# Kernel optimization log

Measured on AMD Instinct MI355X. Metric: run time of the kernel, lower is better.

## Reference

```python
import jax, jax.numpy as jnp
import numpy as np

NTYPES = 2
B, N, MNEI = 4, 512, 100
M = MNEI * NTYPES          # neighbor slots = maxNeighborNum * ntypes
EMB_LAST = 100             # embedding net sizes [25, 50, 100]
FIT_H = 240
M2 = 16
RMIN, RMAX = 0.5, 6.0


def setup_inputs():
    key = jax.random.key(0)
    ks = jax.random.split(key, 24)
    r = jax.random.uniform(ks[0], (B, N, M), minval=0.6, maxval=7.0)
    v = jax.random.normal(ks[1], (B, N, M, 3))
    v = v / jnp.linalg.norm(v, axis=-1, keepdims=True)
    keep = jax.random.uniform(ks[2], (B, N, M)) < 0.7
    ImageDR = jnp.concatenate([r[..., None], r[..., None] * v], axis=-1)
    ImageDR = jnp.where(keep[..., None], ImageDR, 0.0).astype(jnp.float32)
    Imagetype_map = jax.random.randint(ks[3], (N,), 0, NTYPES)
    list_neigh = jax.random.randint(ks[4], (B, N, M), 0, N + 1)
    type_map = jnp.arange(NTYPES)
    davg = (0.01 * jax.random.normal(ks[5], (NTYPES, M, 4))).astype(jnp.float32)
    dstd = (1.0 + 0.1 * jax.random.uniform(ks[6], (NTYPES, M, 4))).astype(jnp.float32)

    def w(k, shape, fan):
        return (jax.random.normal(k, shape) / np.sqrt(fan)).astype(jnp.float32)

    def b(k, shape):
        return (0.1 * jax.random.normal(k, shape)).astype(jnp.float32)

    emb_W0 = w(ks[7], (NTYPES, NTYPES, 1, 25), 1)
    emb_b0 = b(ks[8], (NTYPES, NTYPES, 25))
    emb_W1 = w(ks[9], (NTYPES, NTYPES, 25, 50), 25)
    emb_b1 = b(ks[10], (NTYPES, NTYPES, 50))
    emb_W2 = w(ks[11], (NTYPES, NTYPES, 50, 100), 50)
    emb_b2 = b(ks[12], (NTYPES, NTYPES, 100))
    fin = M2 * EMB_LAST
    fit_W0 = w(ks[13], (NTYPES, fin, FIT_H), fin)
    fit_b0 = b(ks[14], (NTYPES, FIT_H))
    fit_W1 = w(ks[15], (NTYPES, FIT_H, FIT_H), FIT_H)
    fit_b1 = b(ks[16], (NTYPES, FIT_H))
    fit_W2 = w(ks[17], (NTYPES, FIT_H, FIT_H), FIT_H)
    fit_b2 = b(ks[18], (NTYPES, FIT_H))
    fit_W3 = w(ks[19], (NTYPES, FIT_H, 1), FIT_H)
    fit_b3 = b(ks[20], (NTYPES, 1))
    energy_shift = jnp.array([-3.37, -5.21], dtype=jnp.float32)
    return dict(list_neigh=list_neigh, Imagetype_map=Imagetype_map, type_map=type_map,
                ImageDR=ImageDR, nghost=0, davg=davg, dstd=dstd,
                emb_W0=emb_W0, emb_b0=emb_b0, emb_W1=emb_W1, emb_b1=emb_b1,
                emb_W2=emb_W2, emb_b2=emb_b2,
                fit_W0=fit_W0, fit_b0=fit_b0, fit_W1=fit_W1, fit_b1=fit_b1,
                fit_W2=fit_W2, fit_b2=fit_b2, fit_W3=fit_W3, fit_b3=fit_b3,
                energy_shift=energy_shift)


def _emb(s, W0, b0, W1, b1, W2, b2):
    # DeepPot-SE embedding net with doubling resnet connections
    h = jnp.tanh(s @ W0 + b0)                                   # [..., 25]
    h = jnp.tanh(h @ W1 + b1) + jnp.concatenate([h, h], -1)     # [..., 50]
    return jnp.tanh(h @ W2 + b2) + jnp.concatenate([h, h], -1)  # [..., 100]


def _fit(d, W0, b0, W1, b1, W2, b2, W3, b3):
    h = jnp.tanh(d @ W0 + b0)
    h = h + jnp.tanh(h @ W1 + b1)
    h = h + jnp.tanh(h @ W2 + b2)
    return h @ W3 + b3


def _forward(ImageDR, davg, dstd,
             emb_W0, emb_b0, emb_W1, emb_b1, emb_W2, emb_b2,
             fit_W0, fit_b0, fit_W1, fit_b1, fit_W2, fit_b2, fit_W3, fit_b3,
             energy_shift, Imagetype_map):
    Bsz, Nat, Mtot, _ = ImageDR.shape
    m = Mtot // NTYPES
    R = ImageDR[..., 0]
    Rsafe = jnp.where(R > 1e-5, R, 1.0)
    # smooth switching function s(r): 1/r below Rmin, polynomial taper to Rmax
    u = (R - RMIN) / (RMAX - RMIN)
    mid = (u ** 3 * (-6.0 * u * u + 15.0 * u - 10.0) + 1.0) / Rsafe
    S = jnp.where((R > 0) & (R < RMIN), 1.0 / Rsafe,
                  jnp.where((R > RMIN) & (R < RMAX), mid, 0.0))
    msk = (jnp.abs(R) > 1e-5)[..., None]
    Ri = jnp.concatenate([S[..., None],
                          jnp.where(msk, (S / Rsafe)[..., None] * ImageDR[..., 1:4], 0.0)],
                         axis=-1)                                    # [B,N,M,4] = (s, s*x/r, s*y/r, s*z/r)
    # per-center-type normalization (irregular gather of stats)
    Rn = (Ri - davg[Imagetype_map][None]) / dstd[Imagetype_map][None]
    tmask = [(Imagetype_map == i).astype(Rn.dtype)[None, :, None, None] for i in range(NTYPES)]
    xyz = jnp.zeros((Bsz, Nat, 4, EMB_LAST), Rn.dtype)
    for j in range(NTYPES):                                          # neighbor-type slice
        sl = Rn[:, :, j * m:(j + 1) * m, :]                          # [B,N,m,4]
        s = sl[..., 0:1]
        G = jnp.zeros(sl.shape[:3] + (EMB_LAST,), sl.dtype)
        for i in range(NTYPES):                                      # center type -> pair net (i, j)
            G = G + tmask[i] * _emb(s, emb_W0[i, j], emb_b0[i, j],
                                    emb_W1[i, j], emb_b1[i, j], emb_W2[i, j], emb_b2[i, j])
        xyz = xyz + jnp.einsum('bnmk,bnmc->bnkc', sl, G)
    xyz = xyz / (m * NTYPES)
    # descriptor D = (Ri^T G)^T (Ri^T G)[:, :M2], flattened -> [B,N,EMB_LAST*M2]
    D = jnp.einsum('bnkc,bnkd->bncd', xyz, xyz[..., :M2]).reshape(Bsz, Nat, -1)
    Ei = jnp.zeros((Bsz, Nat), D.dtype)
    for i in range(NTYPES):
        e = _fit(D, fit_W0[i], fit_b0[i], fit_W1[i], fit_b1[i],
                 fit_W2[i], fit_b2[i], fit_W3[i], fit_b3[i])[..., 0] + energy_shift[i]
        Ei = Ei + tmask[i][:, :, 0, 0] * e
    Etot = jnp.sum(Ei, axis=1)
    return Etot, Ei


def reference(list_neigh, Imagetype_map, type_map, ImageDR, nghost, davg, dstd,
              emb_W0, emb_b0, emb_W1, emb_b1, emb_W2, emb_b2,
              fit_W0, fit_b0, fit_W1, fit_b1, fit_W2, fit_b2, fit_W3, fit_b3,
              energy_shift):
    return _forward(ImageDR, davg, dstd,
                    emb_W0, emb_b0, emb_W1, emb_b1, emb_W2, emb_b2,
                    fit_W0, fit_b0, fit_W1, fit_b1, fit_W2, fit_b2, fit_W3, fit_b3,
                    energy_shift, Imagetype_map)
```

## Files before the change

### kernel.cpp

```cpp
#include <hip/hip_runtime.h>
#include <math.h>

#define NT 2
#define BSZ 4
#define NAT 512
#define NATOMS 2048
#define NNEI 200
#define EMB 100
#define FITH 240
#define DDIM 1600
#define TBK 1024

#define BIAS_F  16
#define W3C_F   (BIAS_F + 3 * 512)
#define PERM_I  2064
#define CNT_I   (PERM_I + 2048)
#define USH_BYTE 16512
#define TBL_U   0
#define W0T_U   409600
#define W1T_U   (W0T_U + 819200)
#define W2T_U   (W1T_U + 262144)
#define D_U     (W2T_U + 262144)
#define H0_U    (D_U + 3276800)
#define H1_U    (H0_U + 1048576)
#define USH_END (H1_U + 1048576)
#define WS_NEED ((size_t)USH_BYTE + (size_t)USH_END * 2)

#define N_W0 819200
#define N_W1 262144
#define N_W2 262144
#define N_B  1536
#define N_W3 512
#define N_EI 2048
#define N_WT (N_W0 + N_W1 + N_W2 + N_B + N_W3 + N_EI)
#define WT_BLK ((N_WT + 255) / 256)
#define TB_BLK 512

#define HPAD 264

typedef short s8v __attribute__((ext_vector_type(8)));
typedef float f4v __attribute__((ext_vector_type(4)));

__device__ __forceinline__ float ftanh(float x) {
    float ax = fabsf(x);
    float e = __expf(2.0f * ax);
    float t = 1.0f - __fdividef(2.0f, e + 1.0f);
    return (x < 0.0f) ? -t : t;
}
__device__ __forceinline__ unsigned short f2bf(float f) {
    unsigned u = __float_as_uint(f);
    u += 0x7FFFu + ((u >> 16) & 1u);
    return (unsigned short)(u >> 16);
}
__device__ __forceinline__ float bf2f(unsigned short s) {
    return __uint_as_float(((unsigned)s) << 16);
}
__device__ __forceinline__ float calc_S(float R) {
    float Rsafe = (R > 1e-5f) ? R : 1.0f;
    float u = (R - 0.5f) * (1.0f / 5.5f);
    float uu = u * u;
    float mid = (u * uu * (-6.0f * uu + 15.0f * u - 10.0f) + 1.0f) / Rsafe;
    float S = 0.0f;
    if (R > 0.0f && R < 0.5f)      S = 1.0f / Rsafe;
    else if (R > 0.5f && R < 6.0f) S = mid;
    return S;
}

__global__ void __launch_bounds__(256) prep_kernel(
    const float* __restrict__ fW0, const float* __restrict__ fW1,
    const float* __restrict__ fW2,
    const float* __restrict__ fb0, const float* __restrict__ fb1,
    const float* __restrict__ fb2,
    const float* __restrict__ fW3, const float* __restrict__ fb3,
    const float* __restrict__ eshift,
    const float* __restrict__ davg, const float* __restrict__ dstd,
    const float* __restrict__ eW0, const float* __restrict__ eb0,
    const float* __restrict__ eW1, const float* __restrict__ eb1,
    const float* __restrict__ eW2, const float* __restrict__ eb2,
    const int* __restrict__ itype,
    float* __restrict__ ws, float* __restrict__ out)
{
    __shared__ float los[100], his[100];
    __shared__ float rng[2];
    __shared__ float h0s[8][25];
    __shared__ float h1s[8][50];
    __shared__ int pcnt, poff0, poff1;
    const int tid = threadIdx.x;
    int bxg = blockIdx.x;
    unsigned short* u0 = (unsigned short*)((char*)ws + USH_BYTE);

    if (bxg < WT_BLK) {
        int id = bxg * 256 + tid;
        if (id < N_W0) {
            int n = id / 1600, k = id - n * 1600;
            float v = 0.0f;
            if (n < 240)                  v = fW0[(size_t)k * 240 + n];
            else if (n >= 256 && n < 496) v = fW0[(size_t)(1600 + k) * 240 + (n - 256)];
            u0[W0T_U + id] = f2bf(v);
            return;
        }
        id -= N_W0;
        if (id < N_W1) {
            int n = id / 512, k = id - n * 512;
            float v = 0.0f;
            if (n < 240 && k < 240)       v = fW1[(size_t)k * 240 + n];
            else if (n >= 256 && n < 496 && k >= 256 && k < 496)
                                          v = fW1[(size_t)(240 + (k - 256)) * 240 + (n - 256)];
            u0[W1T_U + id] = f2bf(v);
            return;
        }
        id -= N_W1;
        if (id < N_W2) {
            int n = id / 512, k = id - n * 512;
            float v = 0.0f;
            if (n < 240 && k < 240)       v = fW2[(size_t)k * 240 + n];
            else if (n >= 256 && n < 496 && k >= 256 && k < 496)
                                          v = fW2[(size_t)(240 + (k - 256)) * 240 + (n - 256)];
            u0[W2T_U + id] = f2bf(v);
            return;
        }
        id -= N_W2;
        if (id < N_B) {
            int l = id / 512, n = id - l * 512;
            const float* fb = (l == 0) ? fb0 : (l == 1) ? fb1 : fb2;
            float v = 0.0f;
            if (n < 240)                  v = fb[n];
            else if (n >= 256 && n < 496) v = fb[240 + (n - 256)];
            ws[BIAS_F + l * 512 + n] = v;
            return;
        }
        id -= N_B;
        if (id < N_W3) {
            int n = id;
            float v = 0.0f;
            if (n < 240)                  v = fW3[n];
            else if (n >= 256 && n < 496) v = fW3[240 + (n - 256)];
            ws[W3C_F + n] = v;
            return;
        }
        id -= N_W3;
        if (id < N_EI) {
            int t = itype[id & (NAT - 1)];
            out[4 + id] = fb3[t] + eshift[t];
        }
        return;
    }
    bxg -= WT_BLK;
    if (bxg < TB_BLK) {
        const int nid = bxg >> 7;
        const int kb  = (bxg & 127) * 8;
        const int t = nid >> 1, j = nid & 1;
        if (tid < 100) {
            int m = j * 100 + tid;
            float av = davg[(t * NNEI + m) * 4];
            float sd = dstd[(t * NNEI + m) * 4];
            float inv = __fdividef(1.0f, sd);
            float a = (0.0f - av) * inv;
            float b = (2.0f - av) * inv;
            los[tid] = fminf(a, b);
            his[tid] = fmaxf(a, b);
        }
        __syncthreads();
        if (tid == 0) {
            float lo = los[0], hi = his[0];
            for (int i = 1; i < 100; ++i) { lo = fminf(lo, los[i]); hi = fmaxf(hi, his[i]); }
            rng[0] = lo; rng[1] = hi - lo;
            if (kb == 0) {
                ws[nid * 2] = lo;
                ws[nid * 2 + 1] = (float)(TBK - 1) / (hi - lo);
            }
        }
        __syncthreads();
        const float smin = rng[0], span = rng[1];
        const float* W0 = eW0 + nid * 25;
        const float* B0 = eb0 + nid * 25;
        if (tid < 200) {
            int q = tid / 25, a = tid % 25;
            float s = smin + span * ((float)(kb + q) * (1.0f / (TBK - 1)));
            h0s[q][a] = ftanh(fmaf(s, W0[a], B0[a]));
        }
        __syncthreads();
        const float* W1 = eW1 + nid * 1250;
        const float* B1 = eb1 + nid * 50;
        for (int idx = tid; idx < 400; idx += 256) {
            int q = idx / 50, cc = idx % 50;
            float acc = B1[cc];
#pragma unroll
            for (int a = 0; a < 25; ++a) acc = fmaf(h0s[q][a], W1[a * 50 + cc], acc);
            h1s[q][cc] = ftanh(acc) + h0s[q][(cc < 25) ? cc : cc - 25];
        }
        __syncthreads();
        const float* W2 = eW2 + nid * 5000;
        const float* B2 = eb2 + nid * 100;
        unsigned short* tblu = u0 + TBL_U;
        for (int idx = tid; idx < 800; idx += 256) {
            int q = idx / 100, c = idx % 100;
            float acc = B2[c];
#pragma unroll
            for (int a = 0; a < 50; ++a) acc = fmaf(h1s[q][a], W2[a * 100 + c], acc);
            float g = ftanh(acc) + h1s[q][(c < 50) ? c : c - 50];
            tblu[(size_t)(nid * TBK + kb + q) * 100 + c] = f2bf(g);
        }
        return;
    }
    if (tid == 0) { pcnt = 0; poff0 = 0; poff1 = 0; }
    __syncthreads();
    int* wsi = (int*)ws;
    int local0 = 0;
    for (int i = tid; i < NATOMS; i += 256) local0 += (itype[i & (NAT - 1)] == 0);
    atomicAdd(&pcnt, local0);
    __syncthreads();
    const int c0 = pcnt;
    for (int i = tid; i < NATOMS; i += 256) {
        int t = itype[i & (NAT - 1)];
        int pos = (t == 0) ? atomicAdd(&poff0, 1) : (c0 + atomicAdd(&poff1, 1));
        wsi[PERM_I + pos] = i;
    }
    if (tid == 0) { wsi[CNT_I] = c0; wsi[CNT_I + 1] = NATOMS - c0; }
}

__global__ void __launch_bounds__(128) embed_kernel(
    const int* __restrict__ itype, const float* __restrict__ imagedr,
    const float* __restrict__ davg, const float* __restrict__ dstd,
    float* __restrict__ ws)
{
    __shared__ __align__(16) float4 srn[NNEI];
    __shared__ float sx[NNEI];
    __shared__ float part[2][400];
    const int atom = blockIdx.x;
    const int n = atom & (NAT - 1);
    const int tid = threadIdx.x;
    const int t = itype[n];
    unsigned short* u0 = (unsigned short*)((char*)ws + USH_BYTE);

    const float sm0 = ws[(t * 2 + 0) * 2], sc0 = ws[(t * 2 + 0) * 2 + 1];
    const float sm1 = ws[(t * 2 + 1) * 2], sc1 = ws[(t * 2 + 1) * 2 + 1];

    for (int m = tid; m < NNEI; m += 128) {
        float4 dr = ((const float4*)imagedr)[(size_t)atom * NNEI + m];
        float R = dr.x;
        float S = calc_S(R);
        float Rsafe = (R > 1e-5f) ? R : 1.0f;
        float sr = (fabsf(R) > 1e-5f) ? (S / Rsafe) : 0.0f;
        float4 av = ((const float4*)davg)[t * NNEI + m];
        float4 sd = ((const float4*)dstd)[t * NNEI + m];
        float4 rv;
        rv.x = (S         - av.x) / sd.x;
        rv.y = (sr * dr.y - av.y) / sd.y;
        rv.z = (sr * dr.z - av.z) / sd.z;
        rv.w = (sr * dr.w - av.w) / sd.w;
        srn[m] = rv;
        float smin = (m >= 100) ? sm1 : sm0;
        float scal = (m >= 100) ? sc1 : sc0;
        sx[m] = fminf(fmaxf((rv.x - smin) * scal, 0.0f), (float)(TBK - 2) + 0.9999f);
    }
    __syncthreads();

    const int w = tid >> 6, lane = tid & 63;
    const unsigned short* T = u0 + TBL_U + (size_t)(t * 2 + w) * TBK * EMB;
    const bool hi = (lane < 36);
    float xA0 = 0, xA1 = 0, xA2 = 0, xA3 = 0;
    float xB0 = 0, xB1 = 0, xB2 = 0, xB3 = 0;
#pragma unroll 4
    for (int mi = 0; mi < 100; ++mi) {
        int m = w * 100 + mi;
        float4 rv = srn[m];
        float x = sx[m];
        int i = (int)x;
        float f = x - (float)i;
        const unsigned short* Tr = T + (size_t)i * EMB;
        float g0 = bf2f(Tr[lane]);
        float g1 = bf2f(Tr[EMB + lane]);
        float g = fmaf(f, g1 - g0, g0);
        xA0 = fmaf(rv.x, g, xA0); xA1 = fmaf(rv.y, g, xA1);
        xA2 = fmaf(rv.z, g, xA2); xA3 = fmaf(rv.w, g, xA3);
        if (hi) {
            float h0v = bf2f(Tr[64 + lane]);
            float h1v = bf2f(Tr[EMB + 64 + lane]);
            float g2 = fmaf(f, h1v - h0v, h0v);
            xB0 = fmaf(rv.x, g2, xB0); xB1 = fmaf(rv.y, g2, xB1);
            xB2 = fmaf(rv.z, g2, xB2); xB3 = fmaf(rv.w, g2, xB3);
        }
    }
    part[w][0 * 100 + lane] = xA0; part[w][1 * 100 + lane] = xA1;
    part[w][2 * 100 + lane] = xA2; part[w][3 * 100 + lane] = xA3;
    if (hi) {
        part[w][0 * 100 + 64 + lane] = xB0; part[w][1 * 100 + 64 + lane] = xB1;
        part[w][2 * 100 + 64 + lane] = xB2; part[w][3 * 100 + 64 + lane] = xB3;
    }
    __syncthreads();
    const float inv = 1.0f / 200.0f;
    for (int idx = tid; idx < 400; idx += 128)
        part[0][idx] = (part[0][idx] + part[1][idx]) * inv;
    __syncthreads();
    unsigned short* Drow = u0 + D_U + (size_t)atom * DDIM;
    const float* xt = part[0];
    for (int idx = tid; idx < DDIM; idx += 128) {
        int c = idx >> 4, d = idx & 15;
        float s = xt[c] * xt[d] + xt[100 + c] * xt[100 + d]
                + xt[200 + c] * xt[200 + d] + xt[300 + c] * xt[300 + d];
        Drow[idx] = f2bf(s);
    }
}

__device__ __forceinline__ void fit_gemm256(
    const unsigned short* Hsrc, const unsigned short* Bp,
    int h, int mr, int q, f4v acc[4])
{
#pragma unroll
    for (int kt = 0; kt < 4; ++kt) {
        s8v av = *(const s8v*)((const char*)Hsrc
                 + (size_t)mr * (HPAD * 2) + h * 256 + q * 16 + kt * 64);
#pragma unroll
        for (int j = 0; j < 4; ++j) {
            s8v b = *(const s8v*)(Bp + j * 16 * 512 + kt * 32);
            acc[j] = __builtin_amdgcn_mfma_f32_16x16x32_bf16(av, b, acc[j], 0, 0, 0);
        }
    }
}

__global__ void __launch_bounds__(512) fit_kernel(
    const unsigned short* __restrict__ A,
    const unsigned short* __restrict__ W0T,
    const unsigned short* __restrict__ W1T,
    const unsigned short* __restrict__ W2T,
    const float* __restrict__ biases,
    const float* __restrict__ w3c,
    const int* __restrict__ wsi,
    float* __restrict__ out)
{
    __shared__ float lred[4][64][17];
    __shared__ unsigned short Hs0[16 * HPAD];
    __shared__ unsigned short Hs1[16 * HPAD];
    __shared__ float red2[16][4];

    const int z = blockIdx.y;
    const int cnt = wsi[CNT_I + z];
    const int my = blockIdx.x;
    if (my * 16 >= cnt) return;
    const int base = z ? wsi[CNT_I] : 0;
    const int tid = threadIdx.x;
    const int w = tid >> 6, lane = tid & 63;
    const int mr = lane & 15, q = lane >> 4;
    const int wc = w & 3, h = w >> 2;
    const int n0 = z * 256 + wc * 64;
    const int m0 = my * 16;
    const int arow = wsi[PERM_I + base + min(m0 + mr, cnt - 1)];

    {
        const unsigned short* Ap = A   + (size_t)arow * DDIM + h * 800 + q * 8;
        const unsigned short* Bp = W0T + (size_t)(n0 + mr) * DDIM + h * 800 + q * 8;
        f4v a0 = {0,0,0,0}, a1 = {0,0,0,0}, a2 = {0,0,0,0}, a3 = {0,0,0,0};
#pragma unroll 5
        for (int kt = 0; kt < 25; ++kt) {
            s8v av = *(const s8v*)(Ap + kt * 32);
            s8v b0 = *(const s8v*)(Bp + kt * 32);
            s8v b1 = *(const s8v*)(Bp + 16 * DDIM + kt * 32);
            s8v b2 = *(const s8v*)(Bp + 32 * DDIM + kt * 32);
            s8v b3 = *(const s8v*)(Bp + 48 * DDIM + kt * 32);
            a0 = __builtin_amdgcn_mfma_f32_16x16x32_bf16(av, b0, a0, 0, 0, 0);
            a1 = __builtin_amdgcn_mfma_f32_16x16x32_bf16(av, b1, a1, 0, 0, 0);
            a2 = __builtin_amdgcn_mfma_f32_16x16x32_bf16(av, b2, a2, 0, 0, 0);
            a3 = __builtin_amdgcn_mfma_f32_16x16x32_bf16(av, b3, a3, 0, 0, 0);
        }
        if (h == 1) {
#pragma unroll
            for (int r = 0; r < 4; ++r) {
                lred[wc][lane][r]      = a0[r];
                lred[wc][lane][4 + r]  = a1[r];
                lred[wc][lane][8 + r]  = a2[r];
                lred[wc][lane][12 + r] = a3[r];
            }
        }
        __syncthreads();
        if (h == 0) {
#pragma unroll
            for (int j = 0; j < 4; ++j) {
                const float bv = biases[n0 + j * 16 + mr];
                f4v* ap = (j == 0) ? &a0 : (j == 1) ? &a1 : (j == 2) ? &a2 : &a3;
#pragma unroll
                for (int r = 0; r < 4; ++r) {
                    float s = (*ap)[r] + lred[wc][lane][j * 4 + r] + bv;
                    int row = q * 4 + r, col = wc * 64 + j * 16 + mr;
                    Hs0[row * HPAD + col] = f2bf(ftanh(s));
                }
            }
        }
        __syncthreads();
    }

    {
        const unsigned short* Bp = W1T + (size_t)(n0 + mr) * 512 + z * 256 + h * 128 + q * 8;
        f4v acc[4] = {{0,0,0,0},{0,0,0,0},{0,0,0,0},{0,0,0,0}};
        fit_gemm256(Hs0, Bp, h, mr, q, acc);
        if (h == 1) {
#pragma unroll
            for (int j = 0; j < 4; ++j)
#pragma unroll
                for (int r = 0; r < 4; ++r) lred[wc][lane][j * 4 + r] = acc[j][r];
        }
        __syncthreads();
        if (h == 0) {
#pragma unroll
            for (int j = 0; j < 4; ++j) {
                const float bv = biases[512 + n0 + j * 16 + mr];
#pragma unroll
                for (int r = 0; r < 4; ++r) {
                    float s = acc[j][r] + lred[wc][lane][j * 4 + r] + bv;
                    int row = q * 4 + r, col = wc * 64 + j * 16 + mr;
                    float hv = bf2f(Hs0[row * HPAD + col]) + ftanh(s);
                    Hs1[row * HPAD + col] = f2bf(hv);
                }
            }
        }
        __syncthreads();
    }

    {
        const unsigned short* Bp = W2T + (size_t)(n0 + mr) * 512 + z * 256 + h * 128 + q * 8;
        f4v acc[4] = {{0,0,0,0},{0,0,0,0},{0,0,0,0},{0,0,0,0}};
        fit_gemm256(Hs1, Bp, h, mr, q, acc);
        if (h == 1) {
#pragma unroll
            for (int j = 0; j < 4; ++j)
#pragma unroll
                for (int r = 0; r < 4; ++r) lred[wc][lane][j * 4 + r] = acc[j][r];
        }
        __syncthreads();
        if (h == 0) {
            float pr[4] = {0, 0, 0, 0};
#pragma unroll
            for (int j = 0; j < 4; ++j) {
                const int col = n0 + j * 16 + mr;
                const float bv = biases[1024 + col];
                const float wv = w3c[col];
#pragma unroll
                for (int r = 0; r < 4; ++r) {
                    float s = acc[j][r] + lred[wc][lane][j * 4 + r] + bv;
                    int row = q * 4 + r, coll = wc * 64 + j * 16 + mr;
                    float hv = bf2f(Hs1[row * HPAD + coll]) + ftanh(s);
                    pr[r] = fmaf(hv, wv, pr[r]);
                }
            }
#pragma unroll
            for (int r = 0; r < 4; ++r) {
                float p = pr[r];
                p += __shfl_xor(p, 1, 16);
                p += __shfl_xor(p, 2, 16);
                p += __shfl_xor(p, 4, 16);
                p += __shfl_xor(p, 8, 16);
                if (mr == 0) red2[q * 4 + r][wc] = p;
            }
        }
        __syncthreads();
        if (tid < 16 && m0 + tid < cnt) {
            const int orow = wsi[PERM_I + base + m0 + tid];
            out[4 + orow] += red2[tid][0] + red2[tid][1] + red2[tid][2] + red2[tid][3];
        }
    }
}

__global__ void etot_kernel(float* __restrict__ out) {
    const int b = blockIdx.x;
    float s = 0.0f;
    for (int n = threadIdx.x; n < NAT; n += 256) s += out[4 + b * NAT + n];
#pragma unroll
    for (int off = 32; off > 0; off >>= 1) s += __shfl_down(s, off, 64);
    __shared__ float rr[4];
    if ((threadIdx.x & 63) == 0) rr[threadIdx.x >> 6] = s;
    __syncthreads();
    if (threadIdx.x == 0) out[b] = rr[0] + rr[1] + rr[2] + rr[3];
}

__global__ void dp_atom_kernel(
    const int* __restrict__ itype, const float* __restrict__ imagedr,
    const float* __restrict__ davg, const float* __restrict__ dstd,
    const float* __restrict__ eW0, const float* __restrict__ eb0,
    const float* __restrict__ eW1, const float* __restrict__ eb1,
    const float* __restrict__ eW2, const float* __restrict__ eb2,
    const float* __restrict__ fW0, const float* __restrict__ fb0,
    const float* __restrict__ fW1, const float* __restrict__ fb1,
    const float* __restrict__ fW2, const float* __restrict__ fb2,
    const float* __restrict__ fW3, const float* __restrict__ fb3,
    const float* __restrict__ eshift, float* __restrict__ out)
{
    __shared__ __align__(16) float4 rn4[NNEI];
    __shared__ __align__(16) float  xyz[4 * EMB];
    __shared__ __align__(16) float  h0s[100 * 25];
    __shared__ __align__(16) float  smem[100 * 52];
    const int atom = blockIdx.x;
    const int n = atom & (NAT - 1);
    const int tid = threadIdx.x;
    const int t = itype[n];
    for (int m = tid; m < NNEI; m += 256) {
        float4 dr = ((const float4*)imagedr)[(size_t)atom * NNEI + m];
        float R = dr.x;
        float S = calc_S(R);
        float Rsafe = (R > 1e-5f) ? R : 1.0f;
        float sr = (fabsf(R) > 1e-5f) ? (S / Rsafe) : 0.0f;
        float4 av = ((const float4*)davg)[t * NNEI + m];
        float4 sd = ((const float4*)dstd)[t * NNEI + m];
        float4 rv;
        rv.x = (S - av.x) / sd.x; rv.y = (sr * dr.y - av.y) / sd.y;
        rv.z = (sr * dr.z - av.z) / sd.z; rv.w = (sr * dr.w - av.w) / sd.w;
        rn4[m] = rv;
    }
    const int c = tid & 127; const int mh = tid >> 7;
    float xp0 = 0, xp1 = 0, xp2 = 0, xp3 = 0;
    for (int j = 0; j < NT; ++j) {
        const int wb = t * NT + j;
        const float* W0 = eW0 + wb * 25; const float* B0 = eb0 + wb * 25;
        const float* W1 = eW1 + wb * 1250; const float* B1 = eb1 + wb * 50;
        const float* W2 = eW2 + wb * 5000; const float* B2 = eb2 + wb * 100;
        __syncthreads();
        for (int idx = tid; idx < 2500; idx += 256) {
            int m = idx / 25, a = idx - m * 25;
            h0s[idx] = ftanh(fmaf(rn4[j * 100 + m].x, W0[a], B0[a]));
        }
        __syncthreads();
        for (int idx = tid; idx < 5000; idx += 256) {
            int m = idx / 50, cc = idx - m * 50;
            const float* h0m = h0s + m * 25;
            float acc = B1[cc];
#pragma unroll
            for (int a = 0; a < 25; ++a) acc = fmaf(h0m[a], W1[a * 50 + cc], acc);
            smem[m * 52 + cc] = ftanh(acc) + h0m[(cc < 25) ? cc : cc - 25];
        }
        for (int idx = tid; idx < 200; idx += 256)
            smem[(idx >> 1) * 52 + 50 + (idx & 1)] = 0.0f;
        __syncthreads();
        if (c < EMB) {
            float w2c[52];
#pragma unroll
            for (int a = 0; a < 50; ++a) w2c[a] = W2[a * EMB + c];
            w2c[50] = 0; w2c[51] = 0;
            const float bc = B2[c];
            const int sk = (c < 50) ? c : c - 50;
            for (int i = 0; i < 50; ++i) {
                int m = mh * 50 + i;
                const float* h1m = smem + m * 52;
                float acc = bc;
#pragma unroll
                for (int q = 0; q < 13; ++q) {
                    float4 hv = ((const float4*)h1m)[q];
                    acc = fmaf(hv.x, w2c[4 * q], acc); acc = fmaf(hv.y, w2c[4 * q + 1], acc);
                    acc = fmaf(hv.z, w2c[4 * q + 2], acc); acc = fmaf(hv.w, w2c[4 * q + 3], acc);
                }
                float g = ftanh(acc) + h1m[sk];
                float4 rm = rn4[j * 100 + m];
                xp0 = fmaf(rm.x, g, xp0); xp1 = fmaf(rm.y, g, xp1);
                xp2 = fmaf(rm.z, g, xp2); xp3 = fmaf(rm.w, g, xp3);
            }
        }
    }
    __syncthreads();
    const float inv = 1.0f / 200.0f;
    if (mh == 0 && c < EMB) {
        xyz[c] = xp0 * inv; xyz[EMB + c] = xp1 * inv;
        xyz[2 * EMB + c] = xp2 * inv; xyz[3 * EMB + c] = xp3 * inv;
    }
    __syncthreads();
    if (mh == 1 && c < EMB) {
        xyz[c] += xp0 * inv; xyz[EMB + c] += xp1 * inv;
        xyz[2 * EMB + c] += xp2 * inv; xyz[3 * EMB + c] += xp3 * inv;
    }
    __syncthreads();
    float* Dld = smem;
    for (int idx = tid; idx < DDIM; idx += 256) {
        int cc = idx >> 4, d = idx & 15;
        Dld[idx] = xyz[cc] * xyz[d] + xyz[EMB + cc] * xyz[EMB + d]
                 + xyz[2 * EMB + cc] * xyz[2 * EMB + d] + xyz[3 * EMB + cc] * xyz[3 * EMB + d];
    }
    __syncthreads();
    float* hA = smem + DDIM; float* hB = hA + FITH; float* h2 = hB + FITH; float* red = h2 + FITH;
    if (tid < FITH) {
        const float* W = fW0 + (size_t)t * DDIM * FITH;
        float acc = fb0[t * FITH + tid];
        for (int f = 0; f < DDIM; f += 4) {
            float4 dv = *(const float4*)(Dld + f);
            acc = fmaf(dv.x, W[f * FITH + tid], acc); acc = fmaf(dv.y, W[(f + 1) * FITH + tid], acc);
            acc = fmaf(dv.z, W[(f + 2) * FITH + tid], acc); acc = fmaf(dv.w, W[(f + 3) * FITH + tid], acc);
        }
        hA[tid] = ftanh(acc);
    }
    __syncthreads();
    if (tid < FITH) {
        const float* W = fW1 + t * FITH * FITH;
        float acc = fb1[t * FITH + tid];
        for (int f = 0; f < FITH; f += 4) {
            float4 hv = *(const float4*)(hA + f);
            acc = fmaf(hv.x, W[f * FITH + tid], acc); acc = fmaf(hv.y, W[(f + 1) * FITH + tid], acc);
            acc = fmaf(hv.z, W[(f + 2) * FITH + tid], acc); acc = fmaf(hv.w, W[(f + 3) * FITH + tid], acc);
        }
        hB[tid] = hA[tid] + ftanh(acc);
    }
    __syncthreads();
    if (tid < FITH) {
        const float* W = fW2 + t * FITH * FITH;
        float acc = fb2[t * FITH + tid];
        for (int f = 0; f < FITH; f += 4) {
            float4 hv = *(const float4*)(hB + f);
            acc = fmaf(hv.x, W[f * FITH + tid], acc); acc = fmaf(hv.y, W[(f + 1) * FITH + tid], acc);
            acc = fmaf(hv.z, W[(f + 2) * FITH + tid], acc); acc = fmaf(hv.w, W[(f + 3) * FITH + tid], acc);
        }
        h2[tid] = hB[tid] + ftanh(acc);
    }
    __syncthreads();
    float p = (tid < FITH) ? h2[tid] * fW3[t * FITH + tid] : 0.0f;
#pragma unroll
    for (int off = 32; off > 0; off >>= 1) p += __shfl_down(p, off, 64);
    if ((tid & 63) == 0) red[tid >> 6] = p;
    __syncthreads();
    if (tid == 0) out[4 + atom] = red[0] + red[1] + red[2] + red[3] + fb3[t] + eshift[t];
}

extern "C" void kernel_launch(void* const* d_in, const int* in_sizes, int n_in,
                              void* d_out, int out_size, void* d_ws, size_t ws_size,
                              hipStream_t stream) {
    const int*   itype   = (const int*)  d_in[1];
    const float* imagedr = (const float*)d_in[3];
    const float* davg    = (const float*)d_in[5];
    const float* dstd    = (const float*)d_in[6];
    const float* eW0     = (const float*)d_in[7];
    const float* eb0     = (const float*)d_in[8];
    const float* eW1     = (const float*)d_in[9];
    const float* eb1     = (const float*)d_in[10];
    const float* eW2     = (const float*)d_in[11];
    const float* eb2     = (const float*)d_in[12];
    const float* fW0     = (const float*)d_in[13];
    const float* fb0     = (const float*)d_in[14];
    const float* fW1     = (const float*)d_in[15];
    const float* fb1     = (const float*)d_in[16];
    const float* fW2     = (const float*)d_in[17];
    const float* fb2     = (const float*)d_in[18];
    const float* fW3     = (const float*)d_in[19];
    const float* fb3     = (const float*)d_in[20];
    const float* eshift  = (const float*)d_in[21];
    float* out = (float*)d_out;
    float* ws  = (float*)d_ws;

    if (ws_size >= WS_NEED) {
        unsigned short* u0 = (unsigned short*)((char*)ws + USH_BYTE);
        const int* wsi = (const int*)ws;
        prep_kernel<<<WT_BLK + TB_BLK + 1, 256, 0, stream>>>(
            fW0, fW1, fW2, fb0, fb1, fb2, fW3, fb3, eshift,
            davg, dstd, eW0, eb0, eW1, eb1, eW2, eb2, itype, ws, out);
        embed_kernel<<<NATOMS, 128, 0, stream>>>(itype, imagedr, davg, dstd, ws);
        fit_kernel<<<dim3(128, 2), 512, 0, stream>>>(
            u0 + D_U, u0 + W0T_U, u0 + W1T_U, u0 + W2T_U,
            ws + BIAS_F, ws + W3C_F, wsi, out);
        etot_kernel<<<BSZ, 256, 0, stream>>>(out);
    } else {
        dp_atom_kernel<<<NATOMS, 256, 0, stream>>>(itype, imagedr, davg, dstd,
            eW0, eb0, eW1, eb1, eW2, eb2,
            fW0, fb0, fW1, fb1, fW2, fb2, fW3, fb3, eshift, out);
        etot_kernel<<<BSZ, 256, 0, stream>>>(out);
    }
}
```

Measured before the change: 193.7 us.

## Software-prefetch table and weight loads, halve fit row tile to double blocks

```diff
diff --git a/kernel.cpp b/kernel.cpp
--- a/kernel.cpp
+++ b/kernel.cpp
@@ -37,6 +37,8 @@
 #define TB_BLK 512
 
 #define HPAD 264
+#define PF 6
+#define PFE 6
 
 typedef short s8v __attribute__((ext_vector_type(8)));
 typedef float f4v __attribute__((ext_vector_type(4)));
@@ -261,22 +263,41 @@
     const bool hi = (lane < 36);
     float xA0 = 0, xA1 = 0, xA2 = 0, xA3 = 0;
     float xB0 = 0, xB1 = 0, xB2 = 0, xB3 = 0;
-#pragma unroll 4
+
+    float ff[PFE];
+    unsigned short cb[PFE][4];
+#pragma unroll
+    for (int p = 0; p < PFE; ++p) {
+        float x = sx[w * 100 + p];
+        int i = (int)x;
+        ff[p] = x - (float)i;
+        const unsigned short* Tr = T + (size_t)i * EMB;
+        cb[p][0] = Tr[lane];
+        cb[p][1] = Tr[EMB + lane];
+        cb[p][2] = Tr[64 + lane];
+        cb[p][3] = Tr[EMB + 64 + lane];
+    }
+#pragma unroll
     for (int mi = 0; mi < 100; ++mi) {
-        int m = w * 100 + mi;
-        float4 rv = srn[m];
-        float x = sx[m];
-        int i = (int)x;
-        float f = x - (float)i;
-        const unsigned short* Tr = T + (size_t)i * EMB;
-        float g0 = bf2f(Tr[lane]);
-        float g1 = bf2f(Tr[EMB + lane]);
+        const int s = mi % PFE;
+        float4 rv = srn[w * 100 + mi];
+        float f  = ff[s];
+        float g0 = bf2f(cb[s][0]), g1 = bf2f(cb[s][1]);
+        float h0v = bf2f(cb[s][2]), h1v = bf2f(cb[s][3]);
+        if (mi + PFE < 100) {
+            float x = sx[w * 100 + mi + PFE];
+            int i = (int)x;
+            ff[s] = x - (float)i;
+            const unsigned short* Tr = T + (size_t)i * EMB;
+            cb[s][0] = Tr[lane];
+            cb[s][1] = Tr[EMB + lane];
+            cb[s][2] = Tr[64 + lane];
+            cb[s][3] = Tr[EMB + 64 + lane];
+        }
         float g = fmaf(f, g1 - g0, g0);
         xA0 = fmaf(rv.x, g, xA0); xA1 = fmaf(rv.y, g, xA1);
         xA2 = fmaf(rv.z, g, xA2); xA3 = fmaf(rv.w, g, xA3);
         if (hi) {
-            float h0v = bf2f(Tr[64 + lane]);
-            float h1v = bf2f(Tr[EMB + 64 + lane]);
             float g2 = fmaf(f, h1v - h0v, h0v);
             xB0 = fmaf(rv.x, g2, xB0); xB1 = fmaf(rv.y, g2, xB1);
             xB2 = fmaf(rv.z, g2, xB2); xB3 = fmaf(rv.w, g2, xB3);
@@ -300,22 +321,6 @@
         float s = xt[c] * xt[d] + xt[100 + c] * xt[100 + d]
                 + xt[200 + c] * xt[200 + d] + xt[300 + c] * xt[300 + d];
         Drow[idx] = f2bf(s);
-    }
-}
-
-__device__ __forceinline__ void fit_gemm256(
-    const unsigned short* Hsrc, const unsigned short* Bp,
-    int h, int mr, int q, f4v acc[4])
-{
-#pragma unroll
-    for (int kt = 0; kt < 4; ++kt) {
-        s8v av = *(const s8v*)((const char*)Hsrc
-                 + (size_t)mr * (HPAD * 2) + h * 256 + q * 16 + kt * 64);
-#pragma unroll
-        for (int j = 0; j < 4; ++j) {
-            s8v b = *(const s8v*)(Bp + j * 16 * 512 + kt * 32);
-            acc[j] = __builtin_amdgcn_mfma_f32_16x16x32_bf16(av, b, acc[j], 0, 0, 0);
-        }
     }
 }
 
@@ -330,69 +335,108 @@
     float* __restrict__ out)
 {
     __shared__ float lred[4][64][17];
-    __shared__ unsigned short Hs0[16 * HPAD];
-    __shared__ unsigned short Hs1[16 * HPAD];
-    __shared__ float red2[16][4];
+    __shared__ unsigned short Hs0[8 * HPAD];
+    __shared__ unsigned short Hs1[8 * HPAD];
+    __shared__ float red2[8][4];
 
     const int z = blockIdx.y;
     const int cnt = wsi[CNT_I + z];
     const int my = blockIdx.x;
-    if (my * 16 >= cnt) return;
+    if (my * 8 >= cnt) return;
     const int base = z ? wsi[CNT_I] : 0;
     const int tid = threadIdx.x;
     const int w = tid >> 6, lane = tid & 63;
     const int mr = lane & 15, q = lane >> 4;
     const int wc = w & 3, h = w >> 2;
     const int n0 = z * 256 + wc * 64;
-    const int m0 = my * 16;
-    const int arow = wsi[PERM_I + base + min(m0 + mr, cnt - 1)];
-
+    const int m0 = my * 8;
+    const int arow = wsi[PERM_I + base + min(m0 + (mr & 7), cnt - 1)];
+
+    s8v abuf[PF];
+    s8v bbuf[PF][4];
+
+    f4v a0 = {0,0,0,0}, a1 = {0,0,0,0}, a2 = {0,0,0,0}, a3 = {0,0,0,0};
     {
         const unsigned short* Ap = A   + (size_t)arow * DDIM + h * 800 + q * 8;
         const unsigned short* Bp = W0T + (size_t)(n0 + mr) * DDIM + h * 800 + q * 8;
-        f4v a0 = {0,0,0,0}, a1 = {0,0,0,0}, a2 = {0,0,0,0}, a3 = {0,0,0,0};
-#pragma unroll 5
+#pragma unroll
+        for (int p = 0; p < PF; ++p) {
+            abuf[p] = *(const s8v*)(Ap + p * 32);
+#pragma unroll
+            for (int j = 0; j < 4; ++j)
+                bbuf[p][j] = *(const s8v*)(Bp + j * 16 * DDIM + p * 32);
+        }
+#pragma unroll
         for (int kt = 0; kt < 25; ++kt) {
-            s8v av = *(const s8v*)(Ap + kt * 32);
-            s8v b0 = *(const s8v*)(Bp + kt * 32);
-            s8v b1 = *(const s8v*)(Bp + 16 * DDIM + kt * 32);
-            s8v b2 = *(const s8v*)(Bp + 32 * DDIM + kt * 32);
-            s8v b3 = *(const s8v*)(Bp + 48 * DDIM + kt * 32);
+            const int s = kt % PF;
+            s8v av = abuf[s];
+            s8v b0 = bbuf[s][0], b1 = bbuf[s][1], b2 = bbuf[s][2], b3 = bbuf[s][3];
+            if (kt + PF < 25) {
+                abuf[s] = *(const s8v*)(Ap + (kt + PF) * 32);
+#pragma unroll
+                for (int j = 0; j < 4; ++j)
+                    bbuf[s][j] = *(const s8v*)(Bp + j * 16 * DDIM + (kt + PF) * 32);
+            }
             a0 = __builtin_amdgcn_mfma_f32_16x16x32_bf16(av, b0, a0, 0, 0, 0);
             a1 = __builtin_amdgcn_mfma_f32_16x16x32_bf16(av, b1, a1, 0, 0, 0);
             a2 = __builtin_amdgcn_mfma_f32_16x16x32_bf16(av, b2, a2, 0, 0, 0);
             a3 = __builtin_amdgcn_mfma_f32_16x16x32_bf16(av, b3, a3, 0, 0, 0);
         }
-        if (h == 1) {
+    }
+    {
+        const unsigned short* Bp1 = W1T + (size_t)(n0 + mr) * 512 + z * 256 + h * 128 + q * 8;
+#pragma unroll
+        for (int kt = 0; kt < 4; ++kt)
+#pragma unroll
+            for (int j = 0; j < 4; ++j)
+                bbuf[kt][j] = *(const s8v*)(Bp1 + j * 16 * 512 + kt * 32);
+    }
+    if (h == 1) {
+#pragma unroll
+        for (int r = 0; r < 4; ++r) {
+            lred[wc][lane][r]      = a0[r];
+            lred[wc][lane][4 + r]  = a1[r];
+            lred[wc][lane][8 + r]  = a2[r];
+            lred[wc][lane][12 + r] = a3[r];
+        }
+    }
+    __syncthreads();
+    if (h == 0) {
+#pragma unroll
+        for (int j = 0; j < 4; ++j) {
+            const float bv = biases[n0 + j * 16 + mr];
+            f4v* ap = (j == 0) ? &a0 : (j == 1) ? &a1 : (j == 2) ? &a2 : &a3;
 #pragma unroll
             for (int r = 0; r < 4; ++r) {
-                lred[wc][lane][r]      = a0[r];
-                lred[wc][lane][4 + r]  = a1[r];
-                lred[wc][lane][8 + r]  = a2[r];
-                lred[wc][lane][12 + r] = a3[r];
-            }
-        }
-        __syncthreads();
-        if (h == 0) {
-#pragma unroll
-            for (int j = 0; j < 4; ++j) {
-                const float bv = biases[n0 + j * 16 + mr];
-                f4v* ap = (j == 0) ? &a0 : (j == 1) ? &a1 : (j == 2) ? &a2 : &a3;
-#pragma unroll
-                for (int r = 0; r < 4; ++r) {
+                int row = q * 4 + r;
+                if (row < 8) {
                     float s = (*ap)[r] + lred[wc][lane][j * 4 + r] + bv;
-                    int row = q * 4 + r, col = wc * 64 + j * 16 + mr;
+                    int col = wc * 64 + j * 16 + mr;
                     Hs0[row * HPAD + col] = f2bf(ftanh(s));
                 }
             }
         }
-        __syncthreads();
-    }
+    }
+    __syncthreads();
 
     {
-        const unsigned short* Bp = W1T + (size_t)(n0 + mr) * 512 + z * 256 + h * 128 + q * 8;
         f4v acc[4] = {{0,0,0,0},{0,0,0,0},{0,0,0,0},{0,0,0,0}};
-        fit_gemm256(Hs0, Bp, h, mr, q, acc);
+#pragma unroll
+        for (int kt = 0; kt < 4; ++kt) {
+            s8v av = *(const s8v*)((const char*)Hs0
+                     + (size_t)(mr & 7) * (HPAD * 2) + h * 256 + q * 16 + kt * 64);
+#pragma unroll
+            for (int j = 0; j < 4; ++j)
+                acc[j] = __builtin_amdgcn_mfma_f32_16x16x32_bf16(av, bbuf[kt][j], acc[j], 0, 0, 0);
+        }
+        {
+            const unsigned short* Bp2 = W2T + (size_t)(n0 + mr) * 512 + z * 256 + h * 128 + q * 8;
+#pragma unroll
+            for (int kt = 0; kt < 4; ++kt)
+#pragma unroll
+                for (int j = 0; j < 4; ++j)
+                    bbuf[kt][j] = *(const s8v*)(Bp2 + j * 16 * 512 + kt * 32);
+        }
         if (h == 1) {
 #pragma unroll
             for (int j = 0; j < 4; ++j)
@@ -406,10 +450,13 @@
                 const float bv = biases[512 + n0 + j * 16 + mr];
 #pragma unroll
                 for (int r = 0; r < 4; ++r) {
-                    float s = acc[j][r] + lred[wc][lane][j * 4 + r] + bv;
-                    int row = q * 4 + r, col = wc * 64 + j * 16 + mr;
-                    float hv = bf2f(Hs0[row * HPAD + col]) + ftanh(s);
-                    Hs1[row * HPAD + col] = f2bf(hv);
+                    int row = q * 4 + r;
+                    if (row < 8) {
+                        float s = acc[j][r] + lred[wc][lane][j * 4 + r] + bv;
+                        int col = wc * 64 + j * 16 + mr;
+                        float hv = bf2f(Hs0[row * HPAD + col]) + ftanh(s);
+                        Hs1[row * HPAD + col] = f2bf(hv);
+                    }
                 }
             }
         }
@@ -417,9 +464,15 @@
     }
 
     {
-        const unsigned short* Bp = W2T + (size_t)(n0 + mr) * 512 + z * 256 + h * 128 + q * 8;
         f4v acc[4] = {{0,0,0,0},{0,0,0,0},{0,0,0,0},{0,0,0,0}};
-        fit_gemm256(Hs1, Bp, h, mr, q, acc);
+#pragma unroll
+        for (int kt = 0; kt < 4; ++kt) {
+            s8v av = *(const s8v*)((const char*)Hs1
+                     + (size_t)(mr & 7) * (HPAD * 2) + h * 256 + q * 16 + kt * 64);
+#pragma unroll
+            for (int j = 0; j < 4; ++j)
+                acc[j] = __builtin_amdgcn_mfma_f32_16x16x32_bf16(av, bbuf[kt][j], acc[j], 0, 0, 0);
+        }
         if (h == 1) {
 #pragma unroll
             for (int j = 0; j < 4; ++j)
@@ -427,7 +480,7 @@
                 for (int r = 0; r < 4; ++r) lred[wc][lane][j * 4 + r] = acc[j][r];
         }
         __syncthreads();
-        if (h == 0) {
+        if (h == 0 && q < 2) {
             float pr[4] = {0, 0, 0, 0};
 #pragma unroll
             for (int j = 0; j < 4; ++j) {
@@ -453,7 +506,7 @@
             }
         }
         __syncthreads();
-        if (tid < 16 && m0 + tid < cnt) {
+        if (tid < 8 && m0 + tid < cnt) {
             const int orow = wsi[PERM_I + base + m0 + tid];
             out[4 + orow] += red2[tid][0] + red2[tid][1] + red2[tid][2] + red2[tid][3];
         }
@@ -646,7 +699,7 @@
             fW0, fW1, fW2, fb0, fb1, fb2, fW3, fb3, eshift,
             davg, dstd, eW0, eb0, eW1, eb1, eW2, eb2, itype, ws, out);
         embed_kernel<<<NATOMS, 128, 0, stream>>>(itype, imagedr, davg, dstd, ws);
-        fit_kernel<<<dim3(128, 2), 512, 0, stream>>>(
+        fit_kernel<<<dim3(256, 2), 512, 0, stream>>>(
             u0 + D_U, u0 + W0T_U, u0 + W1T_U, u0 + W2T_U,
             ws + BIAS_F, ws + W3C_F, wsi, out);
         etot_kernel<<<BSZ, 256, 0, stream>>>(out);
```

Result: slower. 399.7 us (+106.3%).

## Process 32 atoms per fit block to reuse weight loads across two M-tiles

Applied to the files above, without the earlier changes.

```diff
diff --git a/kernel.cpp b/kernel.cpp
--- a/kernel.cpp
+++ b/kernel.cpp
@@ -303,22 +303,6 @@
     }
 }
 
-__device__ __forceinline__ void fit_gemm256(
-    const unsigned short* Hsrc, const unsigned short* Bp,
-    int h, int mr, int q, f4v acc[4])
-{
-#pragma unroll
-    for (int kt = 0; kt < 4; ++kt) {
-        s8v av = *(const s8v*)((const char*)Hsrc
-                 + (size_t)mr * (HPAD * 2) + h * 256 + q * 16 + kt * 64);
-#pragma unroll
-        for (int j = 0; j < 4; ++j) {
-            s8v b = *(const s8v*)(Bp + j * 16 * 512 + kt * 32);
-            acc[j] = __builtin_amdgcn_mfma_f32_16x16x32_bf16(av, b, acc[j], 0, 0, 0);
-        }
-    }
-}
-
 __global__ void __launch_bounds__(512) fit_kernel(
     const unsigned short* __restrict__ A,
     const unsigned short* __restrict__ W0T,
@@ -329,88 +313,120 @@
     const int* __restrict__ wsi,
     float* __restrict__ out)
 {
-    __shared__ float lred[4][64][17];
-    __shared__ unsigned short Hs0[16 * HPAD];
-    __shared__ unsigned short Hs1[16 * HPAD];
-    __shared__ float red2[16][4];
+    __shared__ float lred[4][64][33];
+    __shared__ unsigned short Hs[32 * HPAD];
+    __shared__ float red2[32][4];
 
     const int z = blockIdx.y;
     const int cnt = wsi[CNT_I + z];
     const int my = blockIdx.x;
-    if (my * 16 >= cnt) return;
+    if (my * 32 >= cnt) return;
     const int base = z ? wsi[CNT_I] : 0;
     const int tid = threadIdx.x;
     const int w = tid >> 6, lane = tid & 63;
     const int mr = lane & 15, q = lane >> 4;
     const int wc = w & 3, h = w >> 2;
     const int n0 = z * 256 + wc * 64;
-    const int m0 = my * 16;
-    const int arow = wsi[PERM_I + base + min(m0 + mr, cnt - 1)];
-
+    const int m0 = my * 32;
+    const int ar0 = wsi[PERM_I + base + min(m0 + mr, cnt - 1)];
+    const int ar1 = wsi[PERM_I + base + min(m0 + 16 + mr, cnt - 1)];
+
+    f4v acc[2][4] = {{{0,0,0,0},{0,0,0,0},{0,0,0,0},{0,0,0,0}},
+                     {{0,0,0,0},{0,0,0,0},{0,0,0,0},{0,0,0,0}}};
     {
-        const unsigned short* Ap = A   + (size_t)arow * DDIM + h * 800 + q * 8;
+        const unsigned short* Ap0 = A + (size_t)ar0 * DDIM + h * 800 + q * 8;
+        const unsigned short* Ap1 = A + (size_t)ar1 * DDIM + h * 800 + q * 8;
         const unsigned short* Bp = W0T + (size_t)(n0 + mr) * DDIM + h * 800 + q * 8;
-        f4v a0 = {0,0,0,0}, a1 = {0,0,0,0}, a2 = {0,0,0,0}, a3 = {0,0,0,0};
 #pragma unroll 5
         for (int kt = 0; kt < 25; ++kt) {
-            s8v av = *(const s8v*)(Ap + kt * 32);
+            s8v av0 = *(const s8v*)(Ap0 + kt * 32);
+            s8v av1 = *(const s8v*)(Ap1 + kt * 32);
             s8v b0 = *(const s8v*)(Bp + kt * 32);
             s8v b1 = *(const s8v*)(Bp + 16 * DDIM + kt * 32);
             s8v b2 = *(const s8v*)(Bp + 32 * DDIM + kt * 32);
             s8v b3 = *(const s8v*)(Bp + 48 * DDIM + kt * 32);
-            a0 = __builtin_amdgcn_mfma_f32_16x16x32_bf16(av, b0, a0, 0, 0, 0);
-            a1 = __builtin_amdgcn_mfma_f32_16x16x32_bf16(av, b1, a1, 0, 0, 0);
-            a2 = __builtin_amdgcn_mfma_f32_16x16x32_bf16(av, b2, a2, 0, 0, 0);
-            a3 = __builtin_amdgcn_mfma_f32_16x16x32_bf16(av, b3, a3, 0, 0, 0);
-        }
-        if (h == 1) {
-#pragma unroll
-            for (int r = 0; r < 4; ++r) {
-                lred[wc][lane][r]      = a0[r];
-                lred[wc][lane][4 + r]  = a1[r];
-                lred[wc][lane][8 + r]  = a2[r];
-                lred[wc][lane][12 + r] = a3[r];
-            }
-        }
-        __syncthreads();
-        if (h == 0) {
-#pragma unroll
-            for (int j = 0; j < 4; ++j) {
-                const float bv = biases[n0 + j * 16 + mr];
-                f4v* ap = (j == 0) ? &a0 : (j == 1) ? &a1 : (j == 2) ? &a2 : &a3;
+            acc[0][0] = __builtin_amdgcn_mfma_f32_16x16x32_bf16(av0, b0, acc[0][0], 0, 0, 0);
+            acc[0][1] = __builtin_amdgcn_mfma_f32_16x16x32_bf16(av0, b1, acc[0][1], 0, 0, 0);
+            acc[0][2] = __builtin_amdgcn_mfma_f32_16x16x32_bf16(av0, b2, acc[0][2], 0, 0, 0);
+            acc[0][3] = __builtin_amdgcn_mfma_f32_16x16x32_bf16(av0, b3, acc[0][3], 0, 0, 0);
+            acc[1][0] = __builtin_amdgcn_mfma_f32_16x16x32_bf16(av1, b0, acc[1][0], 0, 0, 0);
+            acc[1][1] = __builtin_amdgcn_mfma_f32_16x16x32_bf16(av1, b1, acc[1][1], 0, 0, 0);
+            acc[1][2] = __builtin_amdgcn_mfma_f32_16x16x32_bf16(av1, b2, acc[1][2], 0, 0, 0);
+            acc[1][3] = __builtin_amdgcn_mfma_f32_16x16x32_bf16(av1, b3, acc[1][3], 0, 0, 0);
+        }
+    }
+    if (h == 1) {
+#pragma unroll
+        for (int g = 0; g < 2; ++g)
+#pragma unroll
+            for (int j = 0; j < 4; ++j)
+#pragma unroll
+                for (int r = 0; r < 4; ++r)
+                    lred[wc][lane][g * 16 + j * 4 + r] = acc[g][j][r];
+    }
+    __syncthreads();
+    if (h == 0) {
+#pragma unroll
+        for (int j = 0; j < 4; ++j) {
+            const float bv = biases[n0 + j * 16 + mr];
+            const int col = wc * 64 + j * 16 + mr;
+#pragma unroll
+            for (int g = 0; g < 2; ++g)
 #pragma unroll
                 for (int r = 0; r < 4; ++r) {
-                    float s = (*ap)[r] + lred[wc][lane][j * 4 + r] + bv;
-                    int row = q * 4 + r, col = wc * 64 + j * 16 + mr;
-                    Hs0[row * HPAD + col] = f2bf(ftanh(s));
+                    float s = acc[g][j][r] + lred[wc][lane][g * 16 + j * 4 + r] + bv;
+                    int row = g * 16 + q * 4 + r;
+                    Hs[row * HPAD + col] = f2bf(ftanh(s));
                 }
-            }
-        }
-        __syncthreads();
-    }
+        }
+    }
+    __syncthreads();
 
     {
         const unsigned short* Bp = W1T + (size_t)(n0 + mr) * 512 + z * 256 + h * 128 + q * 8;
-        f4v acc[4] = {{0,0,0,0},{0,0,0,0},{0,0,0,0},{0,0,0,0}};
-        fit_gemm256(Hs0, Bp, h, mr, q, acc);
+        f4v ac1[2][4] = {{{0,0,0,0},{0,0,0,0},{0,0,0,0},{0,0,0,0}},
+                         {{0,0,0,0},{0,0,0,0},{0,0,0,0},{0,0,0,0}}};
+#pragma unroll
+        for (int kt = 0; kt < 4; ++kt) {
+            s8v av0 = *(const s8v*)((const char*)Hs + (size_t)mr * (HPAD * 2) + h * 256 + q * 16 + kt * 64);
+            s8v av1 = *(const s8v*)((const char*)Hs + (size_t)(16 + mr) * (HPAD * 2) + h * 256 + q * 16 + kt * 64);
+            s8v b0 = *(const s8v*)(Bp + kt * 32);
+            s8v b1 = *(const s8v*)(Bp + 16 * 512 + kt * 32);
+            s8v b2 = *(const s8v*)(Bp + 32 * 512 + kt * 32);
+            s8v b3 = *(const s8v*)(Bp + 48 * 512 + kt * 32);
+            ac1[0][0] = __builtin_amdgcn_mfma_f32_16x16x32_bf16(av0, b0, ac1[0][0], 0, 0, 0);
+            ac1[0][1] = __builtin_amdgcn_mfma_f32_16x16x32_bf16(av0, b1, ac1[0][1], 0, 0, 0);
+            ac1[0][2] = __builtin_amdgcn_mfma_f32_16x16x32_bf16(av0, b2, ac1[0][2], 0, 0, 0);
+            ac1[0][3] = __builtin_amdgcn_mfma_f32_16x16x32_bf16(av0, b3, ac1[0][3], 0, 0, 0);
+            ac1[1][0] = __builtin_amdgcn_mfma_f32_16x16x32_bf16(av1, b0, ac1[1][0], 0, 0, 0);
+            ac1[1][1] = __builtin_amdgcn_mfma_f32_16x16x32_bf16(av1, b1, ac1[1][1], 0, 0, 0);
+            ac1[1][2] = __builtin_amdgcn_mfma_f32_16x16x32_bf16(av1, b2, ac1[1][2], 0, 0, 0);
+            ac1[1][3] = __builtin_amdgcn_mfma_f32_16x16x32_bf16(av1, b3, ac1[1][3], 0, 0, 0);
+        }
         if (h == 1) {
 #pragma unroll
-            for (int j = 0; j < 4; ++j)
-#pragma unroll
-                for (int r = 0; r < 4; ++r) lred[wc][lane][j * 4 + r] = acc[j][r];
+            for (int g = 0; g < 2; ++g)
+#pragma unroll
+                for (int j = 0; j < 4; ++j)
+#pragma unroll
+                    for (int r = 0; r < 4; ++r)
+                        lred[wc][lane][g * 16 + j * 4 + r] = ac1[g][j][r];
         }
         __syncthreads();
         if (h == 0) {
 #pragma unroll
             for (int j = 0; j < 4; ++j) {
                 const float bv = biases[512 + n0 + j * 16 + mr];
-#pragma unroll
-                for (int r = 0; r < 4; ++r) {
-                    float s = acc[j][r] + lred[wc][lane][j * 4 + r] + bv;
-                    int row = q * 4 + r, col = wc * 64 + j * 16 + mr;
-                    float hv = bf2f(Hs0[row * HPAD + col]) + ftanh(s);
-                    Hs1[row * HPAD + col] = f2bf(hv);
-                }
+                const int col = wc * 64 + j * 16 + mr;
+#pragma unroll
+                for (int g = 0; g < 2; ++g)
+#pragma unroll
+                    for (int r = 0; r < 4; ++r) {
+                        float s = ac1[g][j][r] + lred[wc][lane][g * 16 + j * 4 + r] + bv;
+                        int row = g * 16 + q * 4 + r;
+                        float hv = bf2f(Hs[row * HPAD + col]) + ftanh(s);
+                        Hs[row * HPAD + col] = f2bf(hv);
+                    }
             }
         }
         __syncthreads();
@@ -418,42 +434,67 @@
 
     {
         const unsigned short* Bp = W2T + (size_t)(n0 + mr) * 512 + z * 256 + h * 128 + q * 8;
-        f4v acc[4] = {{0,0,0,0},{0,0,0,0},{0,0,0,0},{0,0,0,0}};
-        fit_gemm256(Hs1, Bp, h, mr, q, acc);
+        f4v ac2[2][4] = {{{0,0,0,0},{0,0,0,0},{0,0,0,0},{0,0,0,0}},
+                         {{0,0,0,0},{0,0,0,0},{0,0,0,0},{0,0,0,0}}};
+#pragma unroll
+        for (int kt = 0; kt < 4; ++kt) {
+            s8v av0 = *(const s8v*)((const char*)Hs + (size_t)mr * (HPAD * 2) + h * 256 + q * 16 + kt * 64);
+            s8v av1 = *(const s8v*)((const char*)Hs + (size_t)(16 + mr) * (HPAD * 2) + h * 256 + q * 16 + kt * 64);
+            s8v b0 = *(const s8v*)(Bp + kt * 32);
+            s8v b1 = *(const s8v*)(Bp + 16 * 512 + kt * 32);
+            s8v b2 = *(const s8v*)(Bp + 32 * 512 + kt * 32);
+            s8v b3 = *(const s8v*)(Bp + 48 * 512 + kt * 32);
+            ac2[0][0] = __builtin_amdgcn_mfma_f32_16x16x32_bf16(av0, b0, ac2[0][0], 0, 0, 0);
+            ac2[0][1] = __builtin_amdgcn_mfma_f32_16x16x32_bf16(av0, b1, ac2[0][1], 0, 0, 0);
+            ac2[0][2] = __builtin_amdgcn_mfma_f32_16x16x32_bf16(av0, b2, ac2[0][2], 0, 0, 0);
+            ac2[0][3] = __builtin_amdgcn_mfma_f32_16x16x32_bf16(av0, b3, ac2[0][3], 0, 0, 0);
+            ac2[1][0] = __builtin_amdgcn_mfma_f32_16x16x32_bf16(av1, b0, ac2[1][0], 0, 0, 0);
+            ac2[1][1] = __builtin_amdgcn_mfma_f32_16x16x32_bf16(av1, b1, ac2[1][1], 0, 0, 0);
+            ac2[1][2] = __builtin_amdgcn_mfma_f32_16x16x32_bf16(av1, b2, ac2[1][2], 0, 0, 0);
+            ac2[1][3] = __builtin_amdgcn_mfma_f32_16x16x32_bf16(av1, b3, ac2[1][3], 0, 0, 0);
+        }
         if (h == 1) {
 #pragma unroll
-            for (int j = 0; j < 4; ++j)
-#pragma unroll
-                for (int r = 0; r < 4; ++r) lred[wc][lane][j * 4 + r] = acc[j][r];
+            for (int g = 0; g < 2; ++g)
+#pragma unroll
+                for (int j = 0; j < 4; ++j)
+#pragma unroll
+                    for (int r = 0; r < 4; ++r)
+                        lred[wc][lane][g * 16 + j * 4 + r] = ac2[g][j][r];
         }
         __syncthreads();
         if (h == 0) {
-            float pr[4] = {0, 0, 0, 0};
+            float pr[2][4] = {{0, 0, 0, 0}, {0, 0, 0, 0}};
 #pragma unroll
             for (int j = 0; j < 4; ++j) {
                 const int col = n0 + j * 16 + mr;
                 const float bv = biases[1024 + col];
                 const float wv = w3c[col];
+                const int coll = wc * 64 + j * 16 + mr;
+#pragma unroll
+                for (int g = 0; g < 2; ++g)
+#pragma unroll
+                    for (int r = 0; r < 4; ++r) {
+                        float s = ac2[g][j][r] + lred[wc][lane][g * 16 + j * 4 + r] + bv;
+                        int row = g * 16 + q * 4 + r;
+                        float hv = bf2f(Hs[row * HPAD + coll]) + ftanh(s);
+                        pr[g][r] = fmaf(hv, wv, pr[g][r]);
+                    }
+            }
+#pragma unroll
+            for (int g = 0; g < 2; ++g)
 #pragma unroll
                 for (int r = 0; r < 4; ++r) {
-                    float s = acc[j][r] + lred[wc][lane][j * 4 + r] + bv;
-                    int row = q * 4 + r, coll = wc * 64 + j * 16 + mr;
-                    float hv = bf2f(Hs1[row * HPAD + coll]) + ftanh(s);
-                    pr[r] = fmaf(hv, wv, pr[r]);
+                    float p = pr[g][r];
+                    p += __shfl_xor(p, 1, 16);
+                    p += __shfl_xor(p, 2, 16);
+                    p += __shfl_xor(p, 4, 16);
+                    p += __shfl_xor(p, 8, 16);
+                    if (mr == 0) red2[g * 16 + q * 4 + r][wc] = p;
                 }
-            }
-#pragma unroll
-            for (int r = 0; r < 4; ++r) {
-                float p = pr[r];
-                p += __shfl_xor(p, 1, 16);
-                p += __shfl_xor(p, 2, 16);
-                p += __shfl_xor(p, 4, 16);
-                p += __shfl_xor(p, 8, 16);
-                if (mr == 0) red2[q * 4 + r][wc] = p;
-            }
-        }
-        __syncthreads();
-        if (tid < 16 && m0 + tid < cnt) {
+        }
+        __syncthreads();
+        if (tid < 32 && m0 + tid < cnt) {
             const int orow = wsi[PERM_I + base + m0 + tid];
             out[4 + orow] += red2[tid][0] + red2[tid][1] + red2[tid][2] + red2[tid][3];
         }
@@ -646,7 +687,7 @@
             fW0, fW1, fW2, fb0, fb1, fb2, fW3, fb3, eshift,
             davg, dstd, eW0, eb0, eW1, eb1, eW2, eb2, itype, ws, out);
         embed_kernel<<<NATOMS, 128, 0, stream>>>(itype, imagedr, davg, dstd, ws);
-        fit_kernel<<<dim3(128, 2), 512, 0, stream>>>(
+        fit_kernel<<<dim3(64, 2), 512, 0, stream>>>(
             u0 + D_U, u0 + W0T_U, u0 + W1T_U, u0 + W2T_U,
             ws + BIAS_F, ws + W3C_F, wsi, out);
         etot_kernel<<<BSZ, 256, 0, stream>>>(out);
```

Result: slower. 205.1 us (+5.9%).
